# Performance work log

Hardware: AMD Instinct MI355X
Metric: run time of the kernel (lower is better)

## Reference

```python
import jax, jax.numpy as jnp
import numpy as np

NC = 151  # number of object classes (VG)
NR = 51   # number of relation classes (VG)


def setup_inputs() -> dict:
    key = jax.random.key(0)
    ks = jax.random.split(key, 10)
    B, N, D = 32, 100, 4096
    H = D // 4
    w = lambda k, shape, fan_in: (jax.random.normal(k, shape, jnp.float32) / np.sqrt(fan_in).astype(np.float32))
    return {
        "encoder_reps": jax.random.normal(ks[0], (B * N, D), jnp.float32),
        "W_comp": w(ks[1], (D, H), D),        # obj_comp Linear (no bias)
        "W_ou1": w(ks[2], (H, H), H),         # ou1 Linear
        "W_ofc": w(ks[3], (H, H), H),         # ofc_u Linear
        "W_decomp": w(ks[4], (H, D), H),      # obj_decomp Linear
        "conv1": w(ks[5], (10, NR, 3, 3), NR * 9),  # Conv2d(51,10,3,pad=1)
        "conv2": w(ks[6], (5, 10, 3, 3), 10 * 9),   # Conv2d(10,5,3,pad=1)
        "conv3": w(ks[7], (1, 5, 1, 1), 5),         # Conv2d(5,1,1)
        "freq_emb": jax.random.normal(ks[8], (NC * NC, NR), jnp.float32) * 0.01,
        "obj_preds": jax.random.randint(ks[9], (B * N,), 0, NC),
        "num_obj": 100,
    }


def reference(encoder_reps, W_comp, W_ou1, W_ofc, W_decomp, conv1, conv2, conv3, freq_emb, obj_preds, num_obj):
    T, D = encoder_reps.shape
    N = num_obj
    B = T // N
    relu = jax.nn.relu
    # obj_comp then per-image ou1 (vectorized over images)
    comp = relu(encoder_reps @ W_comp).reshape(B, N, -1)   # [B,N,H]
    obj_u1 = relu(comp @ W_ou1)                             # [B,N,H]
    # product-index frequency-bias gather: emb[subj*NC + obj]
    labels = obj_preds.reshape(B, N)
    pair_idx = labels[:, :, None] * NC + labels[:, None, :]  # [B,N,N]
    adj_fg = freq_emb[pair_idx]                               # [B,N,N,NR]
    # adjacency net: Conv-Conv-Conv-Tanh over the NxN 'image' with NR channels
    x = jnp.transpose(adj_fg, (0, 3, 1, 2))                   # [B,NR,N,N]
    dn = ("NCHW", "OIHW", "NCHW")
    x = jax.lax.conv_general_dilated(x, conv1, (1, 1), "SAME", dimension_numbers=dn)
    x = jax.lax.conv_general_dilated(x, conv2, (1, 1), "SAME", dimension_numbers=dn)
    x = jnp.tanh(jax.lax.conv_general_dilated(x, conv3, (1, 1), "SAME", dimension_numbers=dn))
    adj = x[:, 0]                                             # [B,N,N]
    # graph message passing: adj @ obj_u1, then ofc_u / decomp + residual
    ofl_u = jnp.einsum("bnm,bmh->bnh", adj, obj_u1).reshape(T, -1)
    u_m = relu(ofl_u @ W_ofc)
    decomp = relu(u_m @ W_decomp)
    return decomp + encoder_reps
```

## Files before the change

kernel.cpp:

```cpp
#include <hip/hip_runtime.h>
#include <cmath>

#define NCC 151
#define NRCH 51
#define BDIM 32
#define NOBJ 100
#define DDIM 4096
#define HDIM 1024
#define TDIM (BDIM * NOBJ)

typedef __bf16 bf16_t;
typedef __bf16 bf16x8 __attribute__((ext_vector_type(8)));
typedef __bf16 bf16x4 __attribute__((ext_vector_type(4)));
typedef float f32x4 __attribute__((ext_vector_type(4)));

template <bool RELU, bool ADDF32OUT, int SPLITK>
__global__ __launch_bounds__(256) void gemm_bf16(
    const bf16_t* __restrict__ A,
    const bf16_t* __restrict__ Bt,
    const float* __restrict__ add,
    void* __restrict__ Cout,
    int N, int K, size_t MN) {
  __shared__ __align__(16) bf16_t Asm[128 * 64];
  __shared__ __align__(16) bf16_t Bsm[128 * 64];
  const int tid = threadIdx.x;
  const int lane = tid & 63;
  const int w = tid >> 6;
  const int wm = w >> 1, wn = w & 1;

  const int nx = gridDim.x, ny = gridDim.y;
  int lin = blockIdx.x + nx * (blockIdx.y + ny * blockIdx.z);
  const int nwg = nx * ny * gridDim.z;
  const int q = nwg >> 3;
  lin = (lin & 7) * q + (lin >> 3);
  const int bx = lin % nx;
  const int r2 = lin / nx;
  const int by = r2 % ny;
  const int bz = r2 / ny;

  const int bm = by * 128, bn = bx * 128;
  const int lr = lane & 15;
  const int lk = lane >> 4;

  int kBeg = 0, kEnd = K;
  if (SPLITK > 1) {
    const int chunk = (((K / 64) + SPLITK - 1) / SPLITK) * 64;
    kBeg = bz * chunk;
    kEnd = min(K, kBeg + chunk);
  }

  f32x4 acc[4][4];
#pragma unroll
  for (int m = 0; m < 4; ++m)
#pragma unroll
    for (int n = 0; n < 4; ++n) acc[m][n] = (f32x4){0.f, 0.f, 0.f, 0.f};

  const int srow = tid >> 3;
  const int sslot = tid & 7;

  char* ldsA = (char*)Asm;
  char* ldsB = (char*)Bsm;

  for (int kt = kBeg; kt < kEnd; kt += 64) {
    __syncthreads();
#pragma unroll
    for (int i = 0; i < 4; ++i) {
      const int row = i * 32 + srow;
      const int kc = sslot ^ (row & 7);
      const bf16_t* ga = A + (size_t)(bm + row) * K + kt + kc * 8;
      const bf16_t* gb = Bt + (size_t)(bn + row) * K + kt + kc * 8;
      __builtin_amdgcn_global_load_lds(
          (const __attribute__((address_space(1))) void*)ga,
          (__attribute__((address_space(3))) void*)(ldsA + i * 4096 + w * 1024),
          16, 0, 0);
      __builtin_amdgcn_global_load_lds(
          (const __attribute__((address_space(1))) void*)gb,
          (__attribute__((address_space(3))) void*)(ldsB + i * 4096 + w * 1024),
          16, 0, 0);
    }
    __syncthreads();

    bf16x8 af[4][2], bfr[4][2];
#pragma unroll
    for (int m = 0; m < 4; ++m) {
      const int row = wm * 64 + m * 16 + lr;
#pragma unroll
      for (int kk = 0; kk < 2; ++kk) {
        const int slot = kk * 4 + lk;
        af[m][kk] =
            *(const bf16x8*)(ldsA + row * 128 + ((slot ^ (lr & 7)) << 4));
      }
    }
#pragma unroll
    for (int n = 0; n < 4; ++n) {
      const int row = wn * 64 + n * 16 + lr;
#pragma unroll
      for (int kk = 0; kk < 2; ++kk) {
        const int slot = kk * 4 + lk;
        bfr[n][kk] =
            *(const bf16x8*)(ldsB + row * 128 + ((slot ^ (lr & 7)) << 4));
      }
    }
#pragma unroll
    for (int m = 0; m < 4; ++m)
#pragma unroll
      for (int n = 0; n < 4; ++n) {
        acc[m][n] = __builtin_amdgcn_mfma_f32_16x16x32_bf16(
            af[m][0], bfr[n][0], acc[m][n], 0, 0, 0);
        acc[m][n] = __builtin_amdgcn_mfma_f32_16x16x32_bf16(
            af[m][1], bfr[n][1], acc[m][n], 0, 0, 0);
      }
  }

  const int or0 = bm + wm * 64 + lk * 4;
  const int oc0 = bn + wn * 64 + lr;
#pragma unroll
  for (int m = 0; m < 4; ++m)
#pragma unroll
    for (int n = 0; n < 4; ++n)
#pragma unroll
      for (int r = 0; r < 4; ++r) {
        float v = acc[m][n][r];
        const size_t off = (size_t)(or0 + m * 16 + r) * N + (oc0 + n * 16);
        if (SPLITK > 1) {
          ((bf16_t*)Cout)[bz * MN + off] = (bf16_t)v;
        } else {
          if (RELU) v = fmaxf(v, 0.f);
          if (ADDF32OUT)
            ((float*)Cout)[off] = v + add[off];
          else
            ((bf16_t*)Cout)[off] = (bf16_t)v;
        }
      }
}

__global__ __launch_bounds__(256) void reduce6_kernel(
    const bf16_t* __restrict__ p, bf16_t* __restrict__ out, int n8,
    size_t MN) {
  int i = blockIdx.x * 256 + threadIdx.x;
  if (i >= n8) return;
  float s[8] = {};
#pragma unroll
  for (int z = 0; z < 6; ++z) {
    bf16x8 v = *(const bf16x8*)(p + z * MN + (size_t)i * 8);
#pragma unroll
    for (int j = 0; j < 8; ++j) s[j] += (float)v[j];
  }
  bf16x8 o;
#pragma unroll
  for (int j = 0; j < 8; ++j) o[j] = (bf16_t)fmaxf(s[j], 0.f);
  *(bf16x8*)(out + (size_t)i * 8) = o;
}

__global__ __launch_bounds__(256) void cvt_bf16_kernel(
    const float* __restrict__ in, bf16_t* __restrict__ out, int n4) {
  int i = blockIdx.x * 256 + threadIdx.x;
  if (i >= n4) return;
  float4 v = ((const float4*)in)[i];
  bf16x4 o = {(bf16_t)v.x, (bf16_t)v.y, (bf16_t)v.z, (bf16_t)v.w};
  ((bf16x4*)out)[i] = o;
}

__global__ __launch_bounds__(256) void transT_kernel(
    const float* __restrict__ in, bf16_t* __restrict__ out, int K, int N) {
  __shared__ float t[32][33];
  const int n0 = blockIdx.x * 32, k0 = blockIdx.y * 32;
  const int tx = threadIdx.x & 31, ty = threadIdx.x >> 5;
#pragma unroll
  for (int i = 0; i < 4; ++i)
    t[ty + i * 8][tx] = in[(size_t)(k0 + ty + i * 8) * N + n0 + tx];
  __syncthreads();
#pragma unroll
  for (int i = 0; i < 4; ++i)
    out[(size_t)(n0 + ty + i * 8) * K + k0 + tx] = (bf16_t)t[tx][ty + i * 8];
}

__global__ __launch_bounds__(256) void prep_w1r_kernel(
    const float* __restrict__ w1, float* __restrict__ w1r) {
  int idx = blockIdx.x * 256 + threadIdx.x;
  if (idx >= NRCH * 90) return;
  int ci = idx / 90, r = idx % 90, k9 = r / 10, co = r % 10;
  w1r[idx] = w1[((co * NRCH + ci) * 3 + k9 / 3) * 3 + (k9 % 3)];
}

__global__ __launch_bounds__(128) void prep_w23_kernel(
    const float* __restrict__ w2, const float* __restrict__ w3,
    float* __restrict__ w23) {
  int t = threadIdx.x;
  if (t >= 90) return;
  int k9 = t / 10, c2 = t % 10;
  float acc = 0.f;
#pragma unroll
  for (int c3 = 0; c3 < 5; ++c3)
    acc += w3[c3] * w2[((c3 * 10 + c2) * 3 + k9 / 3) * 3 + (k9 % 3)];
  w23[t] = acc;
}

__global__ __launch_bounds__(256) void pidx_kernel(
    const int* __restrict__ preds, int* __restrict__ pidx) {
  int idx = blockIdx.x * 256 + threadIdx.x;
  if (idx >= BDIM * NOBJ * NOBJ) return;
  int j = idx % NOBJ;
  int i = (idx / NOBJ) % NOBJ;
  int b = idx / (NOBJ * NOBJ);
  pidx[idx] = preds[b * NOBJ + i] * NCC + preds[b * NOBJ + j];
}

__global__ __launch_bounds__(128) void femb1_kernel(
    const float* __restrict__ femb, const float* __restrict__ w1r,
    float* __restrict__ femb1) {
  __shared__ float row[NRCH];
  const int p = blockIdx.x;
  if (threadIdx.x < NRCH)
    row[threadIdx.x] = femb[(size_t)p * NRCH + threadIdx.x];
  __syncthreads();
  const int t = threadIdx.x;
  if (t >= 90) return;
  float acc = 0.f;
#pragma unroll
  for (int ci = 0; ci < NRCH; ++ci) acc += row[ci] * w1r[ci * 90 + t];
  femb1[((size_t)p * 9 + t / 10) * 12 + (t % 10)] = acc;
}

__global__ __launch_bounds__(256) void conv1g_kernel(
    const int* __restrict__ pidx, const float* __restrict__ femb1,
    float* __restrict__ x1) {
  int idx = blockIdx.x * 256 + threadIdx.x;
  if (idx >= BDIM * NOBJ * NOBJ) return;
  int j = idx % NOBJ;
  int i = (idx / NOBJ) % NOBJ;
  int b = idx / (NOBJ * NOBJ);
  f32x4 a0 = {0.f, 0.f, 0.f, 0.f}, a1 = a0, a2 = a0;
  const int* pb = pidx + b * NOBJ * NOBJ;
#pragma unroll
  for (int kh = 0; kh < 3; ++kh) {
    int ii = i + kh - 1;
    if (ii < 0 || ii >= NOBJ) continue;
#pragma unroll
    for (int kw = 0; kw < 3; ++kw) {
      int jj = j + kw - 1;
      if (jj < 0 || jj >= NOBJ) continue;
      int p = pb[ii * NOBJ + jj];
      const f32x4* f =
          (const f32x4*)(femb1 + ((size_t)p * 9 + kh * 3 + kw) * 12);
      a0 += f[0];
      a1 += f[1];
      a2 += f[2];
    }
  }
  f32x4* o = (f32x4*)(x1 + (size_t)idx * 12);
  o[0] = a0;
  o[1] = a1;
  o[2] = a2;
}

__global__ __launch_bounds__(256) void conv23_kernel(
    const float* __restrict__ x1, const float* __restrict__ w23,
    float* __restrict__ adj) {
  __shared__ float w[90];
  if (threadIdx.x < 90) w[threadIdx.x] = w23[threadIdx.x];
  __syncthreads();
  int idx = blockIdx.x * 256 + threadIdx.x;
  if (idx >= BDIM * NOBJ * NOBJ) return;
  int j = idx % NOBJ;
  int i = (idx / NOBJ) % NOBJ;
  int b = idx / (NOBJ * NOBJ);
  float acc = 0.f;
  const float* xb = x1 + (size_t)b * NOBJ * NOBJ * 12;
#pragma unroll
  for (int kh = 0; kh < 3; ++kh) {
    int ii = i + kh - 1;
    if (ii < 0 || ii >= NOBJ) continue;
#pragma unroll
    for (int kw = 0; kw < 3; ++kw) {
      int jj = j + kw - 1;
      if (jj < 0 || jj >= NOBJ) continue;
      const float* xr = xb + (ii * NOBJ + jj) * 12;
      const float* wr = w + (kh * 3 + kw) * 10;
#pragma unroll
      for (int c = 0; c < 10; ++c) acc += wr[c] * xr[c];
    }
  }
  adj[idx] = tanhf(acc);
}

__global__ __launch_bounds__(256) void einsum_mfma_kernel(
    const float* __restrict__ adj,
    const bf16_t* __restrict__ u1,
    bf16_t* __restrict__ ofl) {
  __shared__ __align__(16) bf16_t As[128 * 128];
  __shared__ __align__(16) bf16_t Us[128 * 128];
  const int b = blockIdx.y;
  const int h0 = blockIdx.x * 128;
  const int tid = threadIdx.x, lane = tid & 63, w = tid >> 6;
  const int wm = w >> 1, wn = w & 1;
  const int lr = lane & 15, lk = lane >> 4;

  {
    f32x4 z = {0.f, 0.f, 0.f, 0.f};
#pragma unroll
    for (int i = 0; i < 8; ++i) ((f32x4*)As)[tid + i * 256] = z;
#pragma unroll
    for (int i = 0; i < 8; ++i) ((f32x4*)Us)[tid + i * 256] = z;
  }
  __syncthreads();

  const float* ab = adj + (size_t)b * 10000;
#pragma unroll
  for (int i = 0; i < 10; ++i) {
    int idx = tid + i * 256;
    if (idx < 2500) {
      int row = idx / 25, kc = idx % 25;
      f32x4 v = ((const f32x4*)ab)[idx];
      bf16x4 o = {(bf16_t)v[0], (bf16_t)v[1], (bf16_t)v[2], (bf16_t)v[3]};
      int slot = kc >> 1;
      *(bf16x4*)((char*)As + row * 256 + ((slot ^ (row & 7)) << 4) +
                 (kc & 1) * 8) = o;
    }
  }

  const bf16_t* ub = u1 + (size_t)b * 100 * HDIM + h0;
#pragma unroll
  for (int i = 0; i < 7; ++i) {
    int idx = tid + i * 256;
    if (idx < 1600) {
      int hc = idx / 100, m = idx % 100;
      bf16x8 v = *(const bf16x8*)(ub + (size_t)m * HDIM + hc * 8);
      int slot = m >> 3, mr = m & 7;
#pragma unroll
      for (int j = 0; j < 8; ++j) {
        int h = hc * 8 + j;
        *((bf16_t*)((char*)Us + h * 256 + ((slot ^ (h & 7)) << 4) + mr * 2)) =
            v[j];
      }
    }
  }
  __syncthreads();

  f32x4 acc[4][4];
#pragma unroll
  for (int m = 0; m < 4; ++m)
#pragma unroll
    for (int n = 0; n < 4; ++n) acc[m][n] = (f32x4){0.f, 0.f, 0.f, 0.f};

#pragma unroll
  for (int ks = 0; ks < 4; ++ks) {
    bf16x8 a[4], u[4];
#pragma unroll
    for (int m = 0; m < 4; ++m) {
      int row = wm * 64 + m * 16 + lr;
      int slot = ks * 4 + lk;
      a[m] = *(const bf16x8*)((char*)As + row * 256 + ((slot ^ (lr & 7)) << 4));
    }
#pragma unroll
    for (int n = 0; n < 4; ++n) {
      int row = wn * 64 + n * 16 + lr;
      int slot = ks * 4 + lk;
      u[n] = *(const bf16x8*)((char*)Us + row * 256 + ((slot ^ (lr & 7)) << 4));
    }
#pragma unroll
    for (int m = 0; m < 4; ++m)
#pragma unroll
      for (int n = 0; n < 4; ++n)
        acc[m][n] =
            __builtin_amdgcn_mfma_f32_16x16x32_bf16(a[m], u[n], acc[m][n], 0, 0, 0);
  }

  const int or0 = wm * 64 + lk * 4;
  const int oc0 = h0 + wn * 64 + lr;
#pragma unroll
  for (int m = 0; m < 4; ++m)
#pragma unroll
    for (int n = 0; n < 4; ++n)
#pragma unroll
      for (int r = 0; r < 4; ++r) {
        int row = or0 + m * 16 + r;
        if (row < 100)
          ofl[((size_t)b * 100 + row) * HDIM + oc0 + n * 16] =
              (bf16_t)acc[m][n][r];
      }
}

extern "C" void kernel_launch(void* const* d_in, const int* in_sizes, int n_in,
                              void* d_out, int out_size, void* d_ws,
                              size_t ws_size, hipStream_t stream) {
  const float* enc = (const float*)d_in[0];
  const float* W_comp = (const float*)d_in[1];
  const float* W_ou1 = (const float*)d_in[2];
  const float* W_ofc = (const float*)d_in[3];
  const float* W_dec = (const float*)d_in[4];
  const float* conv1w = (const float*)d_in[5];
  const float* conv2w = (const float*)d_in[6];
  const float* conv3w = (const float*)d_in[7];
  const float* femb = (const float*)d_in[8];
  const int* preds = (const int*)d_in[9];
  float* out = (float*)d_out;
  char* wsb = (char*)d_ws;

  const size_t MN = (size_t)TDIM * HDIM;

  bf16_t* encb   = (bf16_t*)(wsb + 0);
  bf16_t* WcompT = (bf16_t*)(wsb + 26214400);
  bf16_t* comp   = (bf16_t*)(wsb + 34603008);
  bf16_t* part6  = (bf16_t*)(wsb + 41156608);
  bf16_t* Wou1T  = (bf16_t*)(wsb + 41156608);
  float*  w1r    = (float*)(wsb + 43253760);
  float*  w23    = (float*)(wsb + 43272128);
  float*  femb1  = (float*)(wsb + 43272512);
  int*    pidx   = (int*)(wsb + 53122560);
  float*  x1     = (float*)(wsb + 54402560);
  bf16_t* obj_u1 = (bf16_t*)(wsb + 69762560);
  float*  adj    = (float*)(wsb + 76316160);
  bf16_t* ofl_u  = (bf16_t*)(wsb + 0);
  bf16_t* WofcT  = (bf16_t*)(wsb + 6553600);
  bf16_t* u_m    = (bf16_t*)(wsb + 8650752);
  bf16_t* WdecT  = (bf16_t*)(wsb + 15204352);

  cvt_bf16_kernel<<<(TDIM * DDIM / 4 + 255) / 256, 256, 0, stream>>>(
      enc, encb, TDIM * DDIM / 4);
  transT_kernel<<<dim3(HDIM / 32, DDIM / 32), 256, 0, stream>>>(
      W_comp, WcompT, DDIM, HDIM);

  gemm_bf16<false, false, 6>
      <<<dim3(HDIM / 128, TDIM / 128, 6), 256, 0, stream>>>(
          encb, WcompT, nullptr, part6, HDIM, DDIM, MN);
  reduce6_kernel<<<(int)(MN / 8 / 256), 256, 0, stream>>>(part6, comp,
                                                          (int)(MN / 8), MN);

  transT_kernel<<<dim3(HDIM / 32, HDIM / 32), 256, 0, stream>>>(
      W_ou1, Wou1T, HDIM, HDIM);
  gemm_bf16<true, false, 1>
      <<<dim3(HDIM / 128, TDIM / 128), 256, 0, stream>>>(
          comp, Wou1T, nullptr, obj_u1, HDIM, HDIM, MN);

  prep_w1r_kernel<<<(NRCH * 90 + 255) / 256, 256, 0, stream>>>(conv1w, w1r);
  prep_w23_kernel<<<1, 128, 0, stream>>>(conv2w, conv3w, w23);
  pidx_kernel<<<(BDIM * NOBJ * NOBJ + 255) / 256, 256, 0, stream>>>(preds,
                                                                    pidx);
  femb1_kernel<<<NCC * NCC, 128, 0, stream>>>(femb, w1r, femb1);

  conv1g_kernel<<<(BDIM * NOBJ * NOBJ + 255) / 256, 256, 0, stream>>>(
      pidx, femb1, x1);
  conv23_kernel<<<(BDIM * NOBJ * NOBJ + 255) / 256, 256, 0, stream>>>(x1, w23,
                                                                      adj);

  transT_kernel<<<dim3(HDIM / 32, HDIM / 32), 256, 0, stream>>>(
      W_ofc, WofcT, HDIM, HDIM);
  transT_kernel<<<dim3(DDIM / 32, HDIM / 32), 256, 0, stream>>>(
      W_dec, WdecT, HDIM, DDIM);

  einsum_mfma_kernel<<<dim3(HDIM / 128, BDIM), 256, 0, stream>>>(adj, obj_u1,
                                                                 ofl_u);

  gemm_bf16<true, false, 1>
      <<<dim3(HDIM / 128, TDIM / 128), 256, 0, stream>>>(
          ofl_u, WofcT, nullptr, u_m, HDIM, HDIM, MN);
  gemm_bf16<true, true, 1>
      <<<dim3(DDIM / 128, TDIM / 128), 256, 0, stream>>>(
          u_m, WdecT, enc, out, DDIM, HDIM, MN);
}
```

Measured before the change: 244.0 us.

## Split-K the square GEMMs and use XCD-aware split-K block mapping

Raises the split-K factor of the encoder compression GEMM from 6 to 8. A new block-index mapping places each K-chunk on one XCD-stride slot, so blocks sharing a K-range of A/B are grouped. The two 1024x1024 GEMMs (ou1 and ofc) now run as 3-way split-K with a separate ReLU reduction kernel, to fill more CUs than the 200-block grid did. This costs extra partial-sum writes and reduce passes in bf16, and more workspace overlapping earlier buffers.

```diff
diff --git a/kernel.cpp b/kernel.cpp
--- a/kernel.cpp
+++ b/kernel.cpp
@@ -14,7 +14,7 @@
 typedef __bf16 bf16x4 __attribute__((ext_vector_type(4)));
 typedef float f32x4 __attribute__((ext_vector_type(4)));
 
-template <bool RELU, bool ADDF32OUT, int SPLITK>
+template <bool RELU, bool ADDF32OUT, int SPLITK, int MODE>
 __global__ __launch_bounds__(256) void gemm_bf16(
     const bf16_t* __restrict__ A,
     const bf16_t* __restrict__ Bt,
@@ -28,15 +28,23 @@
   const int w = tid >> 6;
   const int wm = w >> 1, wn = w & 1;
 
-  const int nx = gridDim.x, ny = gridDim.y;
-  int lin = blockIdx.x + nx * (blockIdx.y + ny * blockIdx.z);
-  const int nwg = nx * ny * gridDim.z;
-  const int q = nwg >> 3;
-  lin = (lin & 7) * q + (lin >> 3);
-  const int bx = lin % nx;
-  const int r2 = lin / nx;
-  const int by = r2 % ny;
-  const int bz = r2 / ny;
+  const int nx = gridDim.x, ny = gridDim.y, nz = gridDim.z;
+  const int h = blockIdx.x + nx * (blockIdx.y + ny * blockIdx.z);
+  int bx, by, bz;
+  if (MODE == 1) {
+    bz = h & 7;
+    const int s = h >> 3;
+    by = s % ny;
+    bx = s / ny;
+  } else {
+    const int nwg = nx * ny * nz;
+    const int q = nwg >> 3;
+    const int lin = (h & 7) * q + (h >> 3);
+    by = lin % ny;
+    const int r = lin / ny;
+    bx = r % nx;
+    bz = r / nx;
+  }
 
   const int bm = by * 128, bn = bx * 128;
   const int lr = lane & 15;
@@ -134,14 +142,15 @@
       }
 }
 
-__global__ __launch_bounds__(256) void reduce6_kernel(
+template <int NPART>
+__global__ __launch_bounds__(256) void reduceN_kernel(
     const bf16_t* __restrict__ p, bf16_t* __restrict__ out, int n8,
     size_t MN) {
   int i = blockIdx.x * 256 + threadIdx.x;
   if (i >= n8) return;
   float s[8] = {};
 #pragma unroll
-  for (int z = 0; z < 6; ++z) {
+  for (int z = 0; z < NPART; ++z) {
     bf16x8 v = *(const bf16x8*)(p + z * MN + (size_t)i * 8);
 #pragma unroll
     for (int j = 0; j < 8; ++j) s[j] += (float)v[j];
@@ -362,8 +371,8 @@
     for (int m = 0; m < 4; ++m)
 #pragma unroll
       for (int n = 0; n < 4; ++n)
-        acc[m][n] =
-            __builtin_amdgcn_mfma_f32_16x16x32_bf16(a[m], u[n], acc[m][n], 0, 0, 0);
+        acc[m][n] = __builtin_amdgcn_mfma_f32_16x16x32_bf16(a[m], u[n],
+                                                            acc[m][n], 0, 0, 0);
   }
 
   const int or0 = wm * 64 + lk * 4;
@@ -402,8 +411,10 @@
   bf16_t* encb   = (bf16_t*)(wsb + 0);
   bf16_t* WcompT = (bf16_t*)(wsb + 26214400);
   bf16_t* comp   = (bf16_t*)(wsb + 34603008);
-  bf16_t* part6  = (bf16_t*)(wsb + 41156608);
+  bf16_t* part8  = (bf16_t*)(wsb + 41156608);
   bf16_t* Wou1T  = (bf16_t*)(wsb + 41156608);
+  bf16_t* part3a = (bf16_t*)(wsb + 43253760);
+  bf16_t* part3b = (bf16_t*)(wsb + 43253760);
   float*  w1r    = (float*)(wsb + 43253760);
   float*  w23    = (float*)(wsb + 43272128);
   float*  femb1  = (float*)(wsb + 43272512);
@@ -416,22 +427,24 @@
   bf16_t* u_m    = (bf16_t*)(wsb + 8650752);
   bf16_t* WdecT  = (bf16_t*)(wsb + 15204352);
 
+  const int n8 = (int)(MN / 8);
+
   cvt_bf16_kernel<<<(TDIM * DDIM / 4 + 255) / 256, 256, 0, stream>>>(
       enc, encb, TDIM * DDIM / 4);
   transT_kernel<<<dim3(HDIM / 32, DDIM / 32), 256, 0, stream>>>(
       W_comp, WcompT, DDIM, HDIM);
 
-  gemm_bf16<false, false, 6>
-      <<<dim3(HDIM / 128, TDIM / 128, 6), 256, 0, stream>>>(
-          encb, WcompT, nullptr, part6, HDIM, DDIM, MN);
-  reduce6_kernel<<<(int)(MN / 8 / 256), 256, 0, stream>>>(part6, comp,
-                                                          (int)(MN / 8), MN);
+  gemm_bf16<false, false, 8, 1>
+      <<<dim3(HDIM / 128, TDIM / 128, 8), 256, 0, stream>>>(
+          encb, WcompT, nullptr, part8, HDIM, DDIM, MN);
+  reduceN_kernel<8><<<n8 / 256, 256, 0, stream>>>(part8, comp, n8, MN);
 
   transT_kernel<<<dim3(HDIM / 32, HDIM / 32), 256, 0, stream>>>(
       W_ou1, Wou1T, HDIM, HDIM);
-  gemm_bf16<true, false, 1>
-      <<<dim3(HDIM / 128, TDIM / 128), 256, 0, stream>>>(
-          comp, Wou1T, nullptr, obj_u1, HDIM, HDIM, MN);
+  gemm_bf16<false, false, 3, 0>
+      <<<dim3(HDIM / 128, TDIM / 128, 3), 256, 0, stream>>>(
+          comp, Wou1T, nullptr, part3a, HDIM, HDIM, MN);
+  reduceN_kernel<3><<<n8 / 256, 256, 0, stream>>>(part3a, obj_u1, n8, MN);
 
   prep_w1r_kernel<<<(NRCH * 90 + 255) / 256, 256, 0, stream>>>(conv1w, w1r);
   prep_w23_kernel<<<1, 128, 0, stream>>>(conv2w, conv3w, w23);
@@ -452,10 +465,12 @@
   einsum_mfma_kernel<<<dim3(HDIM / 128, BDIM), 256, 0, stream>>>(adj, obj_u1,
                                                                  ofl_u);
 
-  gemm_bf16<true, false, 1>
-      <<<dim3(HDIM / 128, TDIM / 128), 256, 0, stream>>>(
-          ofl_u, WofcT, nullptr, u_m, HDIM, HDIM, MN);
-  gemm_bf16<true, true, 1>
+  gemm_bf16<false, false, 3, 0>
+      <<<dim3(HDIM / 128, TDIM / 128, 3), 256, 0, stream>>>(
+          ofl_u, WofcT, nullptr, part3b, HDIM, HDIM, MN);
+  reduceN_kernel<3><<<n8 / 256, 256, 0, stream>>>(part3b, u_m, n8, MN);
+
+  gemm_bf16<true, true, 1, 0>
       <<<dim3(DDIM / 128, TDIM / 128), 256, 0, stream>>>(
           u_m, WdecT, enc, out, DDIM, HDIM, MN);
 }
```

Measured after the change: 253.5 us. 3.9% more time.
